# Optimization experiments

Hardware: AMD Instinct MI355X
Metric: run time of the kernel (lower is better)

The kernel has to match this reference:

```python
import jax, jax.numpy as jnp
import numpy as np

V, E, H, T, B = 32000, 256, 512, 64, 64
PAD = 0


def _gru(xg, h0, Whh, bhh, lens):
    """PyTorch-convention GRU. xg: [T,B,3H] precomputed input gates (W_ih x + b_ih).
    lens: [B] or None; if given, hidden state freezes at t >= lens[b] (packed-seq semantics)."""
    def step(h, inp):
        xg_t, t = inp
        hg = h @ Whh.T + bhh
        xr, xz, xn = jnp.split(xg_t, 3, axis=-1)
        hr, hz, hn = jnp.split(hg, 3, axis=-1)
        r = jax.nn.sigmoid(xr + hr)
        z = jax.nn.sigmoid(xz + hz)
        n = jnp.tanh(xn + r * hn)
        h_new = (1.0 - z) * n + z * h
        if lens is not None:
            h_new = jnp.where((t < lens)[:, None], h_new, h)
        return h_new, h_new
    steps = xg.shape[0]
    hT, outs = jax.lax.scan(step, h0, (xg, jnp.arange(steps)))
    return hT, outs


def setup_inputs() -> dict:
    key = jax.random.key(0)
    ks = jax.random.split(key, 13)
    s = 0.05
    return {
        "x": jax.random.randint(ks[0], (T, B), 0, V),
        "x_lens": jnp.maximum(jax.random.randint(ks[1], (B,), 0, T), 1),
        "y": jax.random.randint(ks[2], (T, B), 0, V),
        "emb": jax.random.normal(ks[3], (V, E), dtype=jnp.float32) * s,
        "enc_Wih": jax.random.normal(ks[4], (3 * H, E), dtype=jnp.float32) * s,
        "enc_Whh": jax.random.normal(ks[5], (3 * H, H), dtype=jnp.float32) * s,
        "enc_bih": jnp.zeros((3 * H,), jnp.float32),
        "enc_bhh": jnp.zeros((3 * H,), jnp.float32),
        "dec_Wih": jax.random.normal(ks[6], (3 * H, E), dtype=jnp.float32) * s,
        "dec_Whh": jax.random.normal(ks[7], (3 * H, H), dtype=jnp.float32) * s,
        "dec_bih": jnp.zeros((3 * H,), jnp.float32),
        "dec_bhh": jnp.zeros((3 * H,), jnp.float32),
        "Wout": jax.random.normal(ks[8], (V, H + E), dtype=jnp.float32) * s,
        "bout": jnp.zeros((V,), jnp.float32),
    }


def reference(x, x_lens, y, emb, enc_Wih, enc_Whh, enc_bih, enc_bhh,
              dec_Wih, dec_Whh, dec_bih, dec_bhh, Wout, bout):
    Tx, bs = x.shape
    # ---- encoder (dropout p=0 => identity) ----
    ex = emb[x]                                   # [T,B,E]
    xg = ex @ enc_Wih.T + enc_bih                 # [T,B,3H]
    h0 = jnp.zeros((bs, enc_Whh.shape[1]), emb.dtype)
    z, _ = _gru(xg, h0, enc_Whh, enc_bhh, x_lens)  # final hidden (packed semantics)
    # ---- decoder, fully teacher-forced (tf_ratio=1.0) ----
    ey = emb[y[:-1]]                              # [T-1,B,E]
    yg = ey @ dec_Wih.T + dec_bih
    _, dec_h = _gru(yg, z, dec_Whh, dec_bhh, None)  # [T-1,B,H]
    logits = jnp.concatenate([dec_h, ey], -1) @ Wout.T + bout  # [T-1,B,V]
    vocab = Wout.shape[0]
    dec_out = jnp.concatenate([jnp.zeros((1, bs, vocab), logits.dtype), logits], 0)
    # ---- CrossEntropy(ignore_index=PAD) over positions 1..T-1 ----
    tgt = y[1:].reshape(-1)
    lp = jax.nn.log_softmax(logits.reshape(-1, vocab), axis=-1)
    nll = -jnp.take_along_axis(lp, tgt[:, None], axis=1)[:, 0]
    mask = (tgt != PAD).astype(logits.dtype)
    loss = jnp.sum(nll * mask) / jnp.maximum(jnp.sum(mask), 1.0)
    return dec_out, loss
```

## Files before the change

### kernel.cpp

```cpp
#include <hip/hip_runtime.h>

typedef unsigned short u16;
typedef unsigned long long u64;
typedef __bf16 bf16x8 __attribute__((ext_vector_type(8)));
typedef float f32x4 __attribute__((ext_vector_type(4)));

#define AS1 __attribute__((address_space(1)))
#define AS3 __attribute__((address_space(3)))

__device__ __forceinline__ u16 f2bf(float f) {
  unsigned u = __builtin_bit_cast(unsigned, f);
  unsigned r = (u + 0x7FFFu + ((u >> 16) & 1u)) >> 16;
  return (u16)r;
}
__device__ __forceinline__ float bf2f(u16 h) {
  unsigned u = ((unsigned)h) << 16;
  return __builtin_bit_cast(float, u);
}

__device__ __forceinline__ u64 ld_coh_u64(const u64* p) {
  return __hip_atomic_load(p, __ATOMIC_RELAXED, __HIP_MEMORY_SCOPE_SYSTEM);
}
__device__ __forceinline__ void st_coh_u64(u64* p, u64 v) {
  __hip_atomic_store(p, v, __ATOMIC_RELAXED, __HIP_MEMORY_SCOPE_SYSTEM);
}

constexpr int V = 32000, E = 256, H = 512, T = 64, B = 64;
constexpr int H3 = 3 * H;
constexpr int MP = T * B;
constexpr int MD = (T - 1) * B;
constexpr int KO = H + E;
constexpr long long OUT_LOGITS_OFF = (long long)B * V;
constexpr long long OUT_LOSS_OFF  = (long long)T * B * V;

__global__ __launch_bounds__(256) void cast_weights(
    const float* __restrict__ eW, const float* __restrict__ dW,
    const float* __restrict__ oW,
    u16* __restrict__ eWb, u16* __restrict__ dWb, u16* __restrict__ oWb)
{
  size_t i = (size_t)blockIdx.x * 256 + threadIdx.x;
  const size_t S1 = (size_t)H3 * E;
  if (i < S1) { eWb[i] = f2bf(eW[i]); return; }
  i -= S1;
  if (i < S1) { dWb[i] = f2bf(dW[i]); return; }
  i -= S1;
  if (i < (size_t)V * KO) oWb[i] = f2bf(oW[i]);
}

__global__ __launch_bounds__(256) void gather_emb(
    const int* __restrict__ x, const int* __restrict__ y,
    const float* __restrict__ emb,
    u16* __restrict__ Aenc, u16* __restrict__ Afin)
{
  const int blk = blockIdx.x, e = threadIdx.x;
  if (blk < MP) {
    int tok = x[blk];
    Aenc[(size_t)blk * E + e] = f2bf(emb[(size_t)tok * E + e]);
  } else {
    int m = blk - MP;
    int tok = (m < MD) ? y[m] : 0;
    Afin[(size_t)m * KO + H + e] = f2bf(emb[(size_t)tok * E + e]);
  }
}

__global__ __launch_bounds__(256) void gemm_nt(
    const u16* __restrict__ A, int lda,
    const u16* __restrict__ W, int ldw,
    const float* __restrict__ bias,
    int Kt,
    float* __restrict__ Cf, u16* __restrict__ Cb,
    int ldc, int Mvalid)
{
  __shared__ u16 a_sm[128 * 32];
  __shared__ u16 b_sm[128 * 32];
  const int tid = threadIdx.x;
  const int lane = tid & 63;
  const int w = tid >> 6;
  const int m0 = blockIdx.x * 128;
  const int n0 = blockIdx.y * 128;
  const int srow = lane >> 2;
  const int gc = (lane & 3) ^ ((lane >> 3) & 3);
  const int r = lane & 15;
  const int q = lane >> 4;
  const int cx = (r >> 1) & 3;
  const int wr = w >> 1, wc = w & 1;

  f32x4 acc[4][4] = {};

  for (int kt = 0; kt < Kt; ++kt) {
    const int k0 = kt * 32;
    __syncthreads();
#pragma unroll
    for (int rr = 0; rr < 2; ++rr) {
      const int rbase = w * 32 + rr * 16;
      const u16* gA = A + (size_t)(m0 + rbase + srow) * lda + k0 + gc * 8;
      const u16* gB = W + (size_t)(n0 + rbase + srow) * ldw + k0 + gc * 8;
      __builtin_amdgcn_global_load_lds((const AS1 void*)gA,
                                       (AS3 void*)&a_sm[rbase * 32], 16, 0, 0);
      __builtin_amdgcn_global_load_lds((const AS1 void*)gB,
                                       (AS3 void*)&b_sm[rbase * 32], 16, 0, 0);
    }
    __syncthreads();
    bf16x8 af[4], bfv[4];
#pragma unroll
    for (int i = 0; i < 4; ++i) {
      af[i]  = *(const bf16x8*)&a_sm[(wr * 64 + i * 16 + r) * 32 + ((q ^ cx) * 8)];
      bfv[i] = *(const bf16x8*)&b_sm[(wc * 64 + i * 16 + r) * 32 + ((q ^ cx) * 8)];
    }
#pragma unroll
    for (int i = 0; i < 4; ++i)
#pragma unroll
      for (int j = 0; j < 4; ++j)
        acc[i][j] = __builtin_amdgcn_mfma_f32_16x16x32_bf16(af[i], bfv[j], acc[i][j], 0, 0, 0);
  }

#pragma unroll
  for (int i = 0; i < 4; ++i) {
#pragma unroll
    for (int j = 0; j < 4; ++j) {
      const int n = n0 + wc * 64 + j * 16 + r;
      const float bv = bias ? bias[n] : 0.f;
#pragma unroll
      for (int v = 0; v < 4; ++v) {
        const int m = m0 + wr * 64 + i * 16 + q * 4 + v;
        if (m < Mvalid) {
          const float val = acc[i][j][v] + bv;
          if (Cf) Cf[(size_t)m * ldc + n] = val;
          else    Cb[(size_t)m * ldc + n] = f2bf(val);
        }
      }
    }
  }
}

__global__ __launch_bounds__(256) void gru_kernel(
    const u16* __restrict__ xgates,
    const float* __restrict__ Whh,
    const float* __restrict__ bhh,
    const int* __restrict__ lens,
    const float* __restrict__ h0,
    float* __restrict__ hf0, float* __restrict__ hf1,
    u16* __restrict__ hb0, u16* __restrict__ hb1,
    int steps, unsigned* __restrict__ bar,
    u16* __restrict__ outA)
{
  extern __shared__ char smem[];
  u16* whh_sm = (u16*)smem;
  u16* h_sm   = (u16*)(smem + 48 * 520 * 2);
  float* hg_sm = (float*)(smem + 112 * 520 * 2);

  const int tid = threadIdx.x;
  const int lane = tid & 63;
  const int w = tid >> 6;
  const int jbase = blockIdx.x * 16;
  const int r = lane & 15, q = lane >> 4;

  for (int e = tid; e < 48 * 512; e += 256) {
    int rowl = e >> 9, k = e & 511;
    int g = rowl >> 4, jl = rowl & 15;
    whh_sm[rowl * 520 + k] = f2bf(Whh[(size_t)(g * 512 + jbase + jl) * 512 + k]);
  }

  const int eb  = tid >> 2;
  const int jl0 = (tid & 3) * 4;
  const int jg0 = jbase + jl0;

  {
    u16 hb4[4];
#pragma unroll
    for (int v2 = 0; v2 < 4; ++v2) {
      float v = h0 ? h0[eb * 512 + jg0 + v2] : 0.f;
      hf0[eb * 512 + jg0 + v2] = v;
      hb4[v2] = f2bf(v);
    }
    u64 pack = (u64)hb4[0] | ((u64)hb4[1] << 16) | ((u64)hb4[2] << 32) |
               ((u64)hb4[3] << 48);
    st_coh_u64((u64*)&hb0[eb * 512 + jg0], pack);
  }
  asm volatile("s_waitcnt vmcnt(0)" ::: "memory");
  __syncthreads();
  if (tid == 0) {
    __hip_atomic_fetch_add(bar, 1u, __ATOMIC_RELAXED, __HIP_MEMORY_SCOPE_SYSTEM);
    while (__hip_atomic_load(bar, __ATOMIC_RELAXED, __HIP_MEMORY_SCOPE_SYSTEM) < 32u)
      __builtin_amdgcn_s_sleep(1);
  }
  __syncthreads();

  for (int t = 0; t < steps; ++t) {
    const float* hf_cur = (t & 1) ? hf1 : hf0;
    const u16*   hb_cur = (t & 1) ? hb1 : hb0;
    float*       hf_nxt = (t & 1) ? hf0 : hf1;
    u16*         hb_nxt = (t & 1) ? hb0 : hb1;

    const size_t mrow = (size_t)t * 64 + eb;
    u64 xrv = *(const u64*)&xgates[mrow * 1536 + jg0];
    u64 xzv = *(const u64*)&xgates[mrow * 1536 + 512 + jg0];
    u64 xnv = *(const u64*)&xgates[mrow * 1536 + 1024 + jg0];

    {
      const u64* src = (const u64*)hb_cur;
      u64 v[32];
#pragma unroll
      for (int i = 0; i < 32; ++i) v[i] = ld_coh_u64(src + i * 256 + tid);
#pragma unroll
      for (int i = 0; i < 32; ++i) {
        int c = i * 256 + tid;
        int row = c >> 7, c4 = c & 127;
        *(u64*)&h_sm[row * 520 + c4 * 4] = v[i];
      }
    }
    __syncthreads();

    f32x4 acc[3] = {};
#pragma unroll
    for (int kt = 0; kt < 16; ++kt) {
      bf16x8 a = *(const bf16x8*)&h_sm[(w * 16 + r) * 520 + kt * 32 + q * 8];
#pragma unroll
      for (int g = 0; g < 3; ++g) {
        bf16x8 bb = *(const bf16x8*)&whh_sm[(g * 16 + r) * 520 + kt * 32 + q * 8];
        acc[g] = __builtin_amdgcn_mfma_f32_16x16x32_bf16(a, bb, acc[g], 0, 0, 0);
      }
    }
#pragma unroll
    for (int g = 0; g < 3; ++g)
#pragma unroll
      for (int v = 0; v < 4; ++v)
        hg_sm[((w * 16 + q * 4 + v) * 3 + g) * 16 + r] = acc[g][v];
    __syncthreads();

    {
      u16 hb4[4];
#pragma unroll
      for (int v2 = 0; v2 < 4; ++v2) {
        const int jl = jl0 + v2, jg = jg0 + v2;
        float xr = bf2f((u16)(xrv >> (16 * v2)));
        float xz = bf2f((u16)(xzv >> (16 * v2)));
        float xn = bf2f((u16)(xnv >> (16 * v2)));
        float hr = hg_sm[(eb * 3 + 0) * 16 + jl] + bhh[jg];
        float hz = hg_sm[(eb * 3 + 1) * 16 + jl] + bhh[512 + jg];
        float hn = hg_sm[(eb * 3 + 2) * 16 + jl] + bhh[1024 + jg];
        float rg = 1.f / (1.f + __expf(-(xr + hr)));
        float zg = 1.f / (1.f + __expf(-(xz + hz)));
        float ng = tanhf(xn + rg * hn);
        float hold = hf_cur[eb * 512 + jg];
        float hnew = (1.f - zg) * ng + zg * hold;
        if (lens && t >= lens[eb]) hnew = hold;
        hf_nxt[eb * 512 + jg] = hnew;
        hb4[v2] = f2bf(hnew);
        if (outA) outA[mrow * (size_t)KO + jg] = hb4[v2];
      }
      u64 pack = (u64)hb4[0] | ((u64)hb4[1] << 16) | ((u64)hb4[2] << 32) |
                 ((u64)hb4[3] << 48);
      st_coh_u64((u64*)&hb_nxt[eb * 512 + jg0], pack);
    }

    asm volatile("s_waitcnt vmcnt(0)" ::: "memory");
    __syncthreads();
    if (tid == 0) {
      __hip_atomic_fetch_add(bar, 1u, __ATOMIC_RELAXED, __HIP_MEMORY_SCOPE_SYSTEM);
      const unsigned tgt = 32u * (unsigned)(t + 2);
      while (__hip_atomic_load(bar, __ATOMIC_RELAXED, __HIP_MEMORY_SCOPE_SYSTEM) < tgt)
        __builtin_amdgcn_s_sleep(1);
    }
    __syncthreads();
  }
}

__global__ __launch_bounds__(256) void loss_rows(
    const float* __restrict__ logits, const int* __restrict__ y,
    float* __restrict__ accum)
{
  __shared__ float sm_m[256], sm_s[256];
  const int row = blockIdx.x;
  const float* rp = logits + (size_t)row * V;
  const int tid = threadIdx.x;
  float m = -1e30f, s = 0.f;
  for (int it = 0; it < 32; ++it) {
    int i4 = tid + it * 256;
    if (i4 < V / 4) {
      float4 x = ((const float4*)rp)[i4];
      float mx = fmaxf(fmaxf(x.x, x.y), fmaxf(x.z, x.w));
      float mn = fmaxf(m, mx);
      s = s * __expf(m - mn) + __expf(x.x - mn) + __expf(x.y - mn) +
          __expf(x.z - mn) + __expf(x.w - mn);
      m = mn;
    }
  }
  sm_m[tid] = m; sm_s[tid] = s;
  __syncthreads();
  for (int off = 128; off > 0; off >>= 1) {
    if (tid < off) {
      float m2 = sm_m[tid + off], s2 = sm_s[tid + off];
      float mn = fmaxf(sm_m[tid], m2);
      sm_s[tid] = sm_s[tid] * __expf(sm_m[tid] - mn) + s2 * __expf(m2 - mn);
      sm_m[tid] = mn;
    }
    __syncthreads();
  }
  if (tid == 0) {
    int tgt = y[row + 64];
    float lse = sm_m[0] + __logf(sm_s[0]);
    float nll = lse - rp[tgt];
    if (tgt != 0) {
      atomicAdd(&accum[0], nll);
      atomicAdd(&accum[1], 1.f);
    }
  }
}

__global__ void finalize_loss(const float* __restrict__ accum, float* __restrict__ out) {
  out[0] = accum[0] / fmaxf(accum[1], 1.f);
}

extern "C" void kernel_launch(void* const* d_in, const int* in_sizes, int n_in,
                              void* d_out, int out_size, void* d_ws, size_t ws_size,
                              hipStream_t stream)
{
  const int*   x      = (const int*)d_in[0];
  const int*   x_lens = (const int*)d_in[1];
  const int*   y      = (const int*)d_in[2];
  const float* emb    = (const float*)d_in[3];
  const float* eWih   = (const float*)d_in[4];
  const float* eWhh   = (const float*)d_in[5];
  const float* ebih   = (const float*)d_in[6];
  const float* ebhh   = (const float*)d_in[7];
  const float* dWih   = (const float*)d_in[8];
  const float* dWhh   = (const float*)d_in[9];
  const float* dbih   = (const float*)d_in[10];
  const float* dbhh   = (const float*)d_in[11];
  const float* Wout   = (const float*)d_in[12];
  const float* bout   = (const float*)d_in[13];
  float* out = (float*)d_out;

  char* ws = (char*)d_ws;
  unsigned* cnt  = (unsigned*)(ws + 0);
  float*    accum = (float*)(ws + 8);
  u16*   Aenc = (u16*)(ws + 256);
  u16*   Afin = (u16*)(ws + 2097408);
  u16*   xg   = (u16*)(ws + 8388864);
  u16*   yg   = (u16*)(ws + 20971776);
  u16*   WEb  = (u16*)(ws + 33554688);
  u16*   WDb  = (u16*)(ws + 34341120);
  u16*   WOb  = (u16*)(ws + 35127552);
  float* hEf  = (float*)(ws + 84279552);
  u16*   hEb  = (u16*)(ws + 84541696);
  float* hDf  = (float*)(ws + 84672768);
  u16*   hDb  = (u16*)(ws + 84934912);

  hipMemsetAsync(d_out, 0, (size_t)B * V * sizeof(float), stream);
  hipMemsetAsync(ws, 0, 256, stream);

  cast_weights<<<99072, 256, 0, stream>>>(eWih, dWih, Wout, WEb, WDb, WOb);
  gather_emb<<<2 * MP, 256, 0, stream>>>(x, y, emb, Aenc, Afin);

  gemm_nt<<<dim3(32, 12), 256, 0, stream>>>(Aenc, E, WEb, E, ebih, E / 32,
                                            nullptr, xg, H3, MP);
  gemm_nt<<<dim3(32, 12), 256, 0, stream>>>(Afin + H, KO, WDb, E, dbih, E / 32,
                                            nullptr, yg, H3, MP);

  const size_t gru_lds = (size_t)112 * 520 * 2 + (size_t)64 * 3 * 16 * 4;
  gru_kernel<<<32, 256, gru_lds, stream>>>(xg, eWhh, ebhh, x_lens, nullptr,
      hEf, hEf + 32768, hEb, hEb + 32768, T, cnt + 0, nullptr);
  gru_kernel<<<32, 256, gru_lds, stream>>>(yg, dWhh, dbhh, nullptr, hEf,
      hDf, hDf + 32768, hDb, hDb + 32768, T - 1, cnt + 1, Afin);

  gemm_nt<<<dim3(32, 250), 256, 0, stream>>>(Afin, KO, WOb, KO, bout, KO / 32,
      out + OUT_LOGITS_OFF, nullptr, V, MD);

  loss_rows<<<MD, 256, 0, stream>>>(out + OUT_LOGITS_OFF, y, accum);
  finalize_loss<<<1, 1, 0, stream>>>(accum, out + OUT_LOSS_OFF);
}
```

Measured before the change: 1.926 ms.

## Add specialized 256x256-tile output-projection GEMM with triple-buffered LDS pipeline

Replaces the generic gemm_nt for the large vocabulary projection with a dedicated kernel. It uses 256x256 tiles, 512 threads, direct global-to-LDS loads with an XOR swizzle, a 3-stage prefetch pipeline, block-index swizzling for L2 locality, and nontemporal stores for the logits. The aim is more operand reuse per block and latency hiding on the dominant GEMM. In exchange it uses larger LDS and register footprints, relies on hard-coded shape constants, and pads M to 4096 rows.

```diff
diff --git a/kernel.cpp b/kernel.cpp
--- a/kernel.cpp
+++ b/kernel.cpp
@@ -128,6 +128,105 @@
           if (Cf) Cf[(size_t)m * ldc + n] = val;
           else    Cb[(size_t)m * ldc + n] = f2bf(val);
         }
+      }
+    }
+  }
+}
+
+__global__ __launch_bounds__(512, 2) void gemm_big(
+    const u16* __restrict__ A,
+    const u16* __restrict__ W,
+    const float* __restrict__ bias,
+    float* __restrict__ C)
+{
+  extern __shared__ u16 sm[];
+  const int tid = threadIdx.x;
+  const int lane = tid & 63, w = tid >> 6;
+  const int wr = w >> 2, wc = w & 3;
+  const int r = lane & 15, q = lane >> 4;
+
+  const int bid = blockIdx.x;
+  const int swz = (bid & 7) * 250 + (bid >> 3);
+  const int mt = swz & 15, nt = swz >> 4;
+  const int m0 = mt * 256, n0 = nt * 256;
+
+  const int rowq = tid >> 2;
+  const int gl = (tid & 3) ^ ((tid >> 3) & 3);
+  const u16* gA0 = A + (size_t)(m0 + rowq) * KO + gl * 8;
+  const u16* gA1 = A + (size_t)(m0 + 128 + rowq) * KO + gl * 8;
+  const u16* gW0 = W + (size_t)(n0 + rowq) * KO + gl * 8;
+  const u16* gW1 = W + (size_t)(n0 + 128 + rowq) * KO + gl * 8;
+
+  auto stage = [&](int c, int kt) {
+    u16* ab = sm + c * 16384;
+    u16* bb = ab + 8192;
+    const int k0 = kt * 32;
+    __builtin_amdgcn_global_load_lds((const AS1 void*)(gA0 + k0),
+                                     (AS3 void*)(ab + w * 512), 16, 0, 0);
+    __builtin_amdgcn_global_load_lds((const AS1 void*)(gW0 + k0),
+                                     (AS3 void*)(bb + w * 512), 16, 0, 0);
+    __builtin_amdgcn_global_load_lds((const AS1 void*)(gA1 + k0),
+                                     (AS3 void*)(ab + 4096 + w * 512), 16, 0, 0);
+    __builtin_amdgcn_global_load_lds((const AS1 void*)(gW1 + k0),
+                                     (AS3 void*)(bb + 4096 + w * 512), 16, 0, 0);
+  };
+
+  const int qa = q ^ ((r >> 1) & 3);
+  int aoff[8], boff[4];
+#pragma unroll
+  for (int i = 0; i < 8; ++i) aoff[i] = (wr * 128 + i * 16 + r) * 32 + qa * 8;
+#pragma unroll
+  for (int j = 0; j < 4; ++j) boff[j] = (wc * 64 + j * 16 + r) * 32 + qa * 8;
+
+  f32x4 acc[8][4] = {};
+
+  stage(0, 0);
+  stage(1, 1);
+  stage(2, 2);
+
+  for (int kt = 0; kt < 24; ++kt) {
+    const int c = kt % 3;
+    if (kt < 22)      asm volatile("s_waitcnt vmcnt(8)" ::: "memory");
+    else if (kt < 23) asm volatile("s_waitcnt vmcnt(4)" ::: "memory");
+    else              asm volatile("s_waitcnt vmcnt(0)" ::: "memory");
+    __builtin_amdgcn_s_barrier();
+    __builtin_amdgcn_sched_barrier(0);
+
+    const u16* ab = sm + c * 16384;
+    const u16* bb = ab + 8192;
+    bf16x8 fa[8], fb[4];
+#pragma unroll
+    for (int i = 0; i < 8; ++i) fa[i] = *(const bf16x8*)&ab[aoff[i]];
+#pragma unroll
+    for (int j = 0; j < 4; ++j) fb[j] = *(const bf16x8*)&bb[boff[j]];
+    asm volatile("s_waitcnt lgkmcnt(0)" ::: "memory");
+    __builtin_amdgcn_sched_barrier(0);
+    __builtin_amdgcn_s_barrier();
+    __builtin_amdgcn_sched_barrier(0);
+
+    if (kt + 3 < 24) stage(c, kt + 3);
+
+    __builtin_amdgcn_s_setprio(1);
+#pragma unroll
+    for (int i = 0; i < 8; ++i)
+#pragma unroll
+      for (int j = 0; j < 4; ++j)
+        acc[i][j] = __builtin_amdgcn_mfma_f32_16x16x32_bf16(fa[i], fb[j], acc[i][j], 0, 0, 0);
+    __builtin_amdgcn_s_setprio(0);
+  }
+
+#pragma unroll
+  for (int j = 0; j < 4; ++j) {
+    const int n = n0 + wc * 64 + j * 16 + r;
+    const float bv = bias[n];
+#pragma unroll
+    for (int i = 0; i < 8; ++i) {
+      const int mbase = m0 + wr * 128 + i * 16 + q * 4;
+#pragma unroll
+      for (int v = 0; v < 4; ++v) {
+        const int m = mbase + v;
+        if (m < MD)
+          __builtin_nontemporal_store(acc[i][j][v] + bv, &C[(size_t)m * V + n]);
       }
     }
   }
@@ -364,8 +463,8 @@
   gru_kernel<<<32, 256, gru_lds, stream>>>(yg, dWhh, dbhh, nullptr, hEf,
       hDf, hDf + 32768, hDb, hDb + 32768, T - 1, cnt + 1, Afin);
 
-  gemm_nt<<<dim3(32, 250), 256, 0, stream>>>(Afin, KO, WOb, KO, bout, KO / 32,
-      out + OUT_LOGITS_OFF, nullptr, V, MD);
+  gemm_big<<<2000, 512, 3 * 16384 * sizeof(u16), stream>>>(
+      Afin, WOb, bout, out + OUT_LOGITS_OFF);
 
   loss_rows<<<MD, 256, 0, stream>>>(out + OUT_LOGITS_OFF, y, accum);
   finalize_loss<<<1, 1, 0, stream>>>(accum, out + OUT_LOSS_OFF);
```

Result: faster. 1.843 ms (-4.3%).
